# Kernel tuning notes

Hardware: AMD Instinct MI355X
Metric: run time of the kernel (lower is better)

The kernel has to match this reference:

```python
import jax, jax.numpy as jnp
import numpy as np

VOCAB, D = 10000, 32
QUEUE_LEN = 100


def setup_inputs() -> dict:
    key = jax.random.key(0)
    ks = jax.random.split(key, 8)
    B, T = 64, 1024
    s = 0.1
    return dict(
        inputs=jax.random.randint(ks[0], (B, T), 0, 10000, dtype=jnp.int32),
        emb=jax.random.normal(ks[1], (VOCAB, D), dtype=jnp.float32) * s,
        k_lstm=jax.random.normal(ks[2], (D, 4 * D), dtype=jnp.float32) * s,
        rk_lstm=jax.random.normal(ks[3], (D, 4 * D), dtype=jnp.float32) * s,
        b_lstm=jnp.zeros((4 * D,), dtype=jnp.float32),
        W1=jax.random.normal(ks[4], (D, D), dtype=jnp.float32) * s,
        b1=jnp.zeros((D,), dtype=jnp.float32),
        W2=jax.random.normal(ks[5], (D, 1), dtype=jnp.float32) * s,
        b2=jnp.zeros((1,), dtype=jnp.float32),
    )


def _lstm(x, k, rk, b):
    # Keras LSTM, gate order [i, f, g(cell), o], sigmoid recurrent act, tanh act.
    B, T, D = x.shape
    xg = jnp.einsum('btd,de->bte', x, k) + b  # precompute input projections

    def step(carry, xg_t):
        h, c = carry
        z = xg_t + h @ rk
        i, f, g, o = jnp.split(z, 4, axis=-1)
        c = jax.nn.sigmoid(f) * c + jax.nn.sigmoid(i) * jnp.tanh(g)
        h = jax.nn.sigmoid(o) * jnp.tanh(c)
        return (h, c), h

    init = (jnp.zeros((B, D), x.dtype), jnp.zeros((B, D), x.dtype))
    _, hs = jax.lax.scan(step, init, jnp.swapaxes(xg, 0, 1))  # [T,B,D]
    return jnp.swapaxes(hs, 0, 1)  # [B,T,D]


def _zero_index_queue(x_ids):
    # Vectorized replacement of the (i,j) Python scan: last QUEUE_LEN positions
    # (row-major order) where token==0, as [QUEUE_LEN,2] int32, padded with -1.
    B, T = x_ids.shape
    flat = (x_ids == 0).reshape(-1)
    N = flat.shape[0]
    ridx = jnp.nonzero(flat[::-1], size=QUEUE_LEN, fill_value=-1)[0]
    pos = jnp.where(ridx >= 0, N - 1 - ridx, -1)[::-1]  # ascending, like deque
    ii = jnp.where(pos >= 0, pos // T, -1)
    jj = jnp.where(pos >= 0, pos % T, -1)
    return jnp.stack([ii, jj], axis=-1).astype(jnp.int32)


def _forward_float(x_ids, emb, k_lstm, rk_lstm, b_lstm, W1, b1, W2, b2):
    x = emb[x_ids]                                  # [B,T,D]
    h = _lstm(x, k_lstm, rk_lstm, b_lstm)           # [B,T,D]
    scores = jnp.einsum('btd,bsd->bts', h, h)       # unscaled dot attention
    attn = jax.nn.softmax(scores, axis=-1)
    ctx = jnp.einsum('bts,bsd->btd', attn, h)       # Keras Attention output
    y = jnp.einsum('btd,bte->bde', ctx, h)          # Dot(axes=(1,1)) -> [B,D,D]
    y = jax.nn.relu(y @ W1 + b1)
    return jax.nn.sigmoid(y @ W2 + b2)              # [B,D,1]


def reference(inputs, emb, k_lstm, rk_lstm, b_lstm, W1, b1, W2, b2):
    x_ids = jnp.where(inputs < VOCAB, inputs, 0)
    out = _forward_float(x_ids, emb, k_lstm, rk_lstm, b_lstm, W1, b1, W2, b2)
    return out, _zero_index_queue(x_ids)
```

## Files before the change

kernel.cpp:

```cpp
#include <hip/hip_runtime.h>
#include <math.h>

#define BB 64
#define TT 1024
#define DD 32
#define GG 128
#define VOCABN 10000
#define QLEN 100

typedef short short8 __attribute__((ext_vector_type(8)));
typedef float floatx4 __attribute__((ext_vector_type(4)));
typedef float floatx2 __attribute__((ext_vector_type(2)));
typedef unsigned short u16;

__device__ __forceinline__ float fsig(float x) {
    return __builtin_amdgcn_rcpf(1.0f + __expf(-x));
}
__device__ __forceinline__ float readlane_f(float v, int l) {
    return __int_as_float(__builtin_amdgcn_readlane(__float_as_int(v), l));
}
__device__ __forceinline__ u16 f2bf_rne(float x) {
    unsigned u = __float_as_uint(x);
    u += 0x7FFF + ((u >> 16) & 1);
    return (u16)(u >> 16);
}
__device__ __forceinline__ float bf2f(u16 s) {
    return __uint_as_float(((unsigned)s) << 16);
}
__device__ __forceinline__ floatx2 fma2(float s, floatx2 w, floatx2 acc) {
    return __builtin_elementwise_fma((floatx2){s, s}, w, acc);
}

#define UU 8
__global__
__attribute__((amdgpu_flat_work_group_size(128, 128)))
__attribute__((amdgpu_waves_per_eu(1, 1)))
void k_lstm_scan(const int* __restrict__ ids,
                 const float* __restrict__ emb,
                 const float* __restrict__ klstm,
                 const float* __restrict__ bias,
                 const float* __restrict__ rk,
                 float* __restrict__ hout,
                 u16* __restrict__ hh, u16* __restrict__ hl,
                 u16* __restrict__ th, u16* __restrict__ tl,
                 int* __restrict__ list,
                 float* __restrict__ outq) {
    const int b = blockIdx.x;
    const int tid = threadIdx.x;
    const int wv = tid >> 6;
    const int l = tid & 63;
    if (b >= BB) {
        if (wv != 0) return;
        const int4* v4 = (const int4*)ids;
        const int C4 = (BB * TT) / 4 / 64;
        const int b4 = l * C4;
        int cnt = 0;
#pragma unroll 4
        for (int i = 0; i < C4; ++i) {
            int4 v = v4[b4 + i];
            cnt += (v.x == 0 || (unsigned)v.x >= VOCABN);
            cnt += (v.y == 0 || (unsigned)v.y >= VOCABN);
            cnt += (v.z == 0 || (unsigned)v.z >= VOCABN);
            cnt += (v.w == 0 || (unsigned)v.w >= VOCABN);
        }
        int scan = cnt;
#pragma unroll
        for (int o = 1; o < 64; o <<= 1) {
            int nn = __shfl_up(scan, o);
            if (l >= o) scan += nn;
        }
        const int total = __shfl(scan, 63);
        int off = scan - cnt;
        const int base = l * (C4 * 4);
#pragma unroll 4
        for (int i = 0; i < C4; ++i) {
            int4 v = v4[b4 + i];
            if (v.x == 0 || (unsigned)v.x >= VOCABN) list[off++] = base + 4 * i;
            if (v.y == 0 || (unsigned)v.y >= VOCABN) list[off++] = base + 4 * i + 1;
            if (v.z == 0 || (unsigned)v.z >= VOCABN) list[off++] = base + 4 * i + 2;
            if (v.w == 0 || (unsigned)v.w >= VOCABN) list[off++] = base + 4 * i + 3;
        }
        __threadfence();
        const int Kc = total < QLEN ? total : QLEN;
        for (int t = l; t < QLEN; t += 64) {
            float ii = -1.0f, jj = -1.0f;
            if (t >= QLEN - Kc) {
                int pos = list[total - QLEN + t];
                ii = (float)(pos >> 10);
                jj = (float)(pos & (TT - 1));
            }
            outq[2 * t] = ii;
            outq[2 * t + 1] = jj;
        }
        return;
    }

    __shared__ float ring[2][UU][GG];
    __shared__ __align__(16) float hring[2][UU][DD];
    const int* idsb = ids + b * TT;

    if (wv == 1) {
        const int ja = l, jb = l + 64;
        floatx2 kp[DD];
#pragma unroll
        for (int d2 = 0; d2 < DD; ++d2)
            kp[d2] = (floatx2){klstm[d2 * GG + ja], klstm[d2 * GG + jb]};
        const floatx2 bj = (floatx2){bias[ja], bias[jb]};
        const int dd = l & 31;
        const int u_r = l >> 3, dc = (l & 7) * 4;
        const int d_c = l & 31, ug = (l >> 5) * 4;
        u16* hhb = hh + (size_t)b * TT * DD;
        u16* hlb = hl + (size_t)b * TT * DD;
        u16* thb = th + (size_t)b * DD * TT;
        u16* tlb = tl + (size_t)b * DD * TT;

#define PROD_TOKEN(SEL, U, EV)                                               \
        {                                                                    \
            floatx2 z0 = bj;                                                 \
            floatx2 z1 = {0.f, 0.f}, z2 = {0.f, 0.f}, z3 = {0.f, 0.f};       \
            _Pragma("unroll")                                                \
            for (int k = 0; k < DD; k += 4) {                                \
                float e0 = readlane_f(EV, k);                                \
                float e1 = readlane_f(EV, k + 1);                            \
                float e2 = readlane_f(EV, k + 2);                            \
                float e3 = readlane_f(EV, k + 3);                            \
                z0 = fma2(e0, kp[k], z0);                                    \
                z1 = fma2(e1, kp[k + 1], z1);                                \
                z2 = fma2(e2, kp[k + 2], z2);                                \
                z3 = fma2(e3, kp[k + 3], z3);                                \
            }                                                                \
            floatx2 zf = (z0 + z1) + (z2 + z3);                              \
            ring[SEL][U][ja] = zf.x;                                         \
            ring[SEL][U][jb] = zf.y;                                         \
        }

#define CVT_CHUNK(HSEL, TC0)                                                 \
        {                                                                    \
            const float4 hv4 = *(const float4*)&hring[HSEL][u_r][dc];        \
            float xr[4] = {hv4.x, hv4.y, hv4.z, hv4.w};                      \
            u16 rh[4], rl[4];                                                \
            _Pragma("unroll")                                                \
            for (int i = 0; i < 4; ++i) {                                    \
                rh[i] = f2bf_rne(xr[i]);                                     \
                rl[i] = f2bf_rne(xr[i] - bf2f(rh[i]));                       \
            }                                                                \
            ushort4 rhv = {rh[0], rh[1], rh[2], rh[3]};                      \
            ushort4 rlv = {rl[0], rl[1], rl[2], rl[3]};                      \
            *(ushort4*)&hhb[(size_t)((TC0) + u_r) * DD + dc] = rhv;          \
            *(ushort4*)&hlb[(size_t)((TC0) + u_r) * DD + dc] = rlv;          \
            u16 ch[4], cl[4];                                                \
            _Pragma("unroll")                                                \
            for (int j = 0; j < 4; ++j) {                                    \
                float x = hring[HSEL][ug + j][d_c];                          \
                ch[j] = f2bf_rne(x);                                         \
                cl[j] = f2bf_rne(x - bf2f(ch[j]));                           \
            }                                                                \
            ushort4 chv = {ch[0], ch[1], ch[2], ch[3]};                      \
            ushort4 clv = {cl[0], cl[1], cl[2], cl[3]};                      \
            *(ushort4*)&thb[(size_t)d_c * TT + (TC0) + ug] = chv;            \
            *(ushort4*)&tlb[(size_t)d_c * TT + (TC0) + ug] = clv;            \
        }

        {
            int id0 = idsb[0]; if ((unsigned)id0 >= VOCABN) id0 = 0;
            float ec = emb[id0 * DD + dd];
#pragma unroll
            for (int u = 0; u < UU; ++u) {
                float en = 0.f;
                if (u + 1 < UU) {
                    int idn = idsb[u + 1]; if ((unsigned)idn >= VOCABN) idn = 0;
                    en = emb[idn * DD + dd];
                }
                PROD_TOKEN(0, u, ec)
                ec = en;
            }
        }
        __syncthreads();
        int sel = 0;
        for (int t0 = 0; t0 < TT; t0 += UU) {
            if (t0 + UU < TT) {
                const int s = sel ^ 1;
                int id0 = idsb[t0 + UU]; if ((unsigned)id0 >= VOCABN) id0 = 0;
                float ec = emb[id0 * DD + dd];
#pragma unroll
                for (int u = 0; u < UU; ++u) {
                    float en = 0.f;
                    if (u + 1 < UU) {
                        int tn = t0 + UU + u + 1;
                        if (tn > TT - 1) tn = TT - 1;
                        int idn = idsb[tn]; if ((unsigned)idn >= VOCABN) idn = 0;
                        en = emb[idn * DD + dd];
                    }
                    PROD_TOKEN(s, u, ec)
                    ec = en;
                }
            }
            if (t0) CVT_CHUNK((t0 / UU - 1) & 1, t0 - UU)
            __syncthreads();
            sel ^= 1;
        }
        CVT_CHUNK(1, TT - UU)
#undef PROD_TOKEN
#undef CVT_CHUNK
        return;
    }

    const int d = l & 31;
    const bool hi = l >= 32;
    const int ga = (hi ? 32 : 0) + d;
    const int gb = (hi ? 96 : 64) + d;
    floatx2 rkp[DD];
#pragma unroll
    for (int k = 0; k < DD; ++k)
        rkp[k] = (floatx2){rk[k * GG + ga], rk[k * GG + gb]};
    float* hb = hout + (size_t)b * TT * DD;

    float h = 0.0f, c = 0.0f;
    float hreg[UU];
    __syncthreads();
    int sel = 0;
    for (int t0 = 0; t0 < TT; t0 += UU) {
        if (t0 && !hi) {
#pragma unroll
            for (int u = 0; u < UU; ++u) hb[(size_t)(t0 - UU + u) * DD + d] = hreg[u];
        }
        float pa[UU], pb[UU];
#pragma unroll
        for (int u = 0; u < UU; ++u) {
            pa[u] = ring[sel][u][ga];
            pb[u] = ring[sel][u][gb];
        }
#pragma unroll
        for (int u = 0; u < UU; ++u) {
            floatx2 x0 = {pa[u], pb[u]};
            floatx2 x1 = {0.f, 0.f}, x2 = {0.f, 0.f}, x3 = {0.f, 0.f};
#pragma unroll
            for (int k = 0; k < DD; k += 4) {
                float h0 = readlane_f(h, k);
                float h1 = readlane_f(h, k + 1);
                float h2 = readlane_f(h, k + 2);
                float h3 = readlane_f(h, k + 3);
                x0 = fma2(h0, rkp[k],     x0);
                x1 = fma2(h1, rkp[k + 1], x1);
                x2 = fma2(h2, rkp[k + 2], x2);
                x3 = fma2(h3, rkp[k + 3], x3);
            }
            floatx2 zf = (x0 + x1) + (x2 + x3);
            float za = zf.x, zb = zf.y;
            float a = fsig(za);
            float zbm = hi ? zb : 2.0f * zb;
            float s2 = fsig(zbm);
            float bv = hi ? s2 : 2.0f * s2 - 1.0f;
            auto r1 = __builtin_amdgcn_permlane32_swap(
                __float_as_int(bv), __float_as_int(a), false, false);
            auto r2 = __builtin_amdgcn_permlane32_swap(
                __float_as_int(a), __float_as_int(bv), false, false);
            float fg = __int_as_float(r1[0]);
            float og = __int_as_float(r2[0]);
            c = fmaf(fg, c, a * bv);
            float tc = 2.0f * fsig(2.0f * c) - 1.0f;
            h = og * tc;
            hreg[u] = h;
            if (!hi) hring[sel][u][d] = h;
        }
        __syncthreads();
        sel ^= 1;
    }
    if (!hi) {
#pragma unroll
        for (int u = 0; u < UU; ++u) hb[(size_t)(TT - UU + u) * DD + d] = hreg[u];
    }
}

__global__ __launch_bounds__(256, 1) void k_attn(const u16* __restrict__ hh,
                                                 const u16* __restrict__ hl,
                                                 const u16* __restrict__ th,
                                                 const u16* __restrict__ tl,
                                                 u16* __restrict__ cth,
                                                 u16* __restrict__ ctl) {
    __shared__ u16 plds[4][4][2][16 * 40];
    const int tid = threadIdx.x;
    const int w = tid >> 6;
    const int l = tid & 63;
    const int m = l & 15;
    const int g = l >> 4;
    const int b = blockIdx.x & 63;
    const int qt = (blockIdx.x >> 6) * 4 + w;
    const int q0 = qt * 64;
    const size_t rb = (size_t)b * TT * DD;
    const size_t tb = (size_t)b * DD * TT;

    const short8 Qh0 = *(const short8*)&hh[rb + (size_t)(q0 + m) * DD + g * 8];
    const short8 Ql0 = *(const short8*)&hl[rb + (size_t)(q0 + m) * DD + g * 8];
    const short8 Qh1 = *(const short8*)&hh[rb + (size_t)(q0 + 16 + m) * DD + g * 8];
    const short8 Ql1 = *(const short8*)&hl[rb + (size_t)(q0 + 16 + m) * DD + g * 8];
    const short8 Qh2 = *(const short8*)&hh[rb + (size_t)(q0 + 32 + m) * DD + g * 8];
    const short8 Ql2 = *(const short8*)&hl[rb + (size_t)(q0 + 32 + m) * DD + g * 8];
    const short8 Qh3 = *(const short8*)&hh[rb + (size_t)(q0 + 48 + m) * DD + g * 8];
    const short8 Ql3 = *(const short8*)&hl[rb + (size_t)(q0 + 48 + m) * DD + g * 8];
    short8 ONES;
#pragma unroll
    for (int j = 0; j < 8; ++j) ONES[j] = (short)0x3F80;

    floatx4 c0 = {0.f, 0.f, 0.f, 0.f}, c1 = {0.f, 0.f, 0.f, 0.f};
    floatx4 c2 = {0.f, 0.f, 0.f, 0.f}, c3 = {0.f, 0.f, 0.f, 0.f};
    floatx4 c4 = {0.f, 0.f, 0.f, 0.f}, c5 = {0.f, 0.f, 0.f, 0.f};
    floatx4 c6 = {0.f, 0.f, 0.f, 0.f}, c7 = {0.f, 0.f, 0.f, 0.f};
    floatx4 la0 = {0.f, 0.f, 0.f, 0.f}, la1 = {0.f, 0.f, 0.f, 0.f};
    floatx4 la2 = {0.f, 0.f, 0.f, 0.f}, la3 = {0.f, 0.f, 0.f, 0.f};

#define S_BLOCK(QH, QL, KH_A, KL_A, KH_B, KL_B, SA, SB)                       \
    SA = __builtin_amdgcn_mfma_f32_16x16x32_bf16(QH, KH_A, SA, 0, 0, 0);      \
    SA = __builtin_amdgcn_mfma_f32_16x16x32_bf16(QH, KL_A, SA, 0, 0, 0);      \
    SA = __builtin_amdgcn_mfma_f32_16x16x32_bf16(QL, KH_A, SA, 0, 0, 0);      \
    SB = __builtin_amdgcn_mfma_f32_16x16x32_bf16(QH, KH_B, SB, 0, 0, 0);      \
    SB = __builtin_amdgcn_mfma_f32_16x16x32_bf16(QH, KL_B, SB, 0, 0, 0);      \
    SB = __builtin_amdgcn_mfma_f32_16x16x32_bf16(QL, KH_B, SB, 0, 0, 0);

#define EXP_STORE(SA, SB, TILE, SLOT)                                         \
    {                                                                         \
        u16* lp = plds[w][TILE][SLOT];                                        \
        _Pragma("unroll")                                                     \
        for (int r = 0; r < 4; ++r) {                                         \
            lp[(g * 4 + r) * 40 + m]      = f2bf_rne(__expf(SA[r]));          \
            lp[(g * 4 + r) * 40 + 16 + m] = f2bf_rne(__expf(SB[r]));          \
        }                                                                     \
    }

    {
        short8 KhA = *(const short8*)&hh[rb + (size_t)(m) * DD + g * 8];
        short8 KlA = *(const short8*)&hl[rb + (size_t)(m) * DD + g * 8];
        short8 KhB = *(const short8*)&hh[rb + (size_t)(16 + m) * DD + g * 8];
        short8 KlB = *(const short8*)&hl[rb + (size_t)(16 + m) * DD + g * 8];
        floatx4 sA = {0.f, 0.f, 0.f, 0.f}, sB = {0.f, 0.f, 0.f, 0.f};
        floatx4 tA = {0.f, 0.f, 0.f, 0.f}, tB = {0.f, 0.f, 0.f, 0.f};
        floatx4 uA = {0.f, 0.f, 0.f, 0.f}, uB = {0.f, 0.f, 0.f, 0.f};
        floatx4 vA = {0.f, 0.f, 0.f, 0.f}, vB = {0.f, 0.f, 0.f, 0.f};
        S_BLOCK(Qh0, Ql0, KhA, KlA, KhB, KlB, sA, sB)
        S_BLOCK(Qh1, Ql1, KhA, KlA, KhB, KlB, tA, tB)
        S_BLOCK(Qh2, Ql2, KhA, KlA, KhB, KlB, uA, uB)
        S_BLOCK(Qh3, Ql3, KhA, KlA, KhB, KlB, vA, vB)
        EXP_STORE(sA, sB, 0, 0)
        EXP_STORE(tA, tB, 1, 0)
        EXP_STORE(uA, uB, 2, 0)
        EXP_STORE(vA, vB, 3, 0)
    }
    short8 Vh0 = *(const short8*)&th[tb + (size_t)m * TT + g * 8];
    short8 Vl0 = *(const short8*)&tl[tb + (size_t)m * TT + g * 8];
    short8 Vh1 = *(const short8*)&th[tb + (size_t)(16 + m) * TT + g * 8];
    short8 Vl1 = *(const short8*)&tl[tb + (size_t)(16 + m) * TT + g * 8];
    short8 KhA = *(const short8*)&hh[rb + (size_t)(32 + m) * DD + g * 8];
    short8 KlA = *(const short8*)&hl[rb + (size_t)(32 + m) * DD + g * 8];
    short8 KhB = *(const short8*)&hh[rb + (size_t)(48 + m) * DD + g * 8];
    short8 KlB = *(const short8*)&hl[rb + (size_t)(48 + m) * DD + g * 8];

#pragma unroll 1
    for (int kp = 1; kp < 32; ++kp) {
        const int knK = (kp < 31) ? (kp + 1) * 32 : 0;
        const int knV = kp * 32;
        short8 nKhA = *(const short8*)&hh[rb + (size_t)(knK + m) * DD + g * 8];
        short8 nKlA = *(const short8*)&hl[rb + (size_t)(knK + m) * DD + g * 8];
        short8 nKhB = *(const short8*)&hh[rb + (size_t)(knK + 16 + m) * DD + g * 8];
        short8 nKlB = *(const short8*)&hl[rb + (size_t)(knK + 16 + m) * DD + g * 8];
        short8 nVh0 = *(const short8*)&th[tb + (size_t)m * TT + knV + g * 8];
        short8 nVl0 = *(const short8*)&tl[tb + (size_t)m * TT + knV + g * 8];
        short8 nVh1 = *(const short8*)&th[tb + (size_t)(16 + m) * TT + knV + g * 8];
        short8 nVl1 = *(const short8*)&tl[tb + (size_t)(16 + m) * TT + knV + g * 8];

        floatx4 sA = {0.f, 0.f, 0.f, 0.f}, sB = {0.f, 0.f, 0.f, 0.f};
        floatx4 tA = {0.f, 0.f, 0.f, 0.f}, tB = {0.f, 0.f, 0.f, 0.f};
        floatx4 uA = {0.f, 0.f, 0.f, 0.f}, uB = {0.f, 0.f, 0.f, 0.f};
        floatx4 vA = {0.f, 0.f, 0.f, 0.f}, vB = {0.f, 0.f, 0.f, 0.f};
        S_BLOCK(Qh0, Ql0, KhA, KlA, KhB, KlB, sA, sB)
        S_BLOCK(Qh1, Ql1, KhA, KlA, KhB, KlB, tA, tB)
        S_BLOCK(Qh2, Ql2, KhA, KlA, KhB, KlB, uA, uB)
        S_BLOCK(Qh3, Ql3, KhA, KlA, KhB, KlB, vA, vB)

        const int ps = (kp - 1) & 1;
        const short8 P0 = *(const short8*)&plds[w][0][ps][m * 40 + g * 8];
        const short8 P1 = *(const short8*)&plds[w][1][ps][m * 40 + g * 8];
        const short8 P2 = *(const short8*)&plds[w][2][ps][m * 40 + g * 8];
        const short8 P3 = *(const short8*)&plds[w][3][ps][m * 40 + g * 8];

        c0  = __builtin_amdgcn_mfma_f32_16x16x32_bf16(P0, Vh0, c0, 0, 0, 0);
        c0  = __builtin_amdgcn_mfma_f32_16x16x32_bf16(P0, Vl0, c0, 0, 0, 0);
        c1  = __builtin_amdgcn_mfma_f32_16x16x32_bf16(P0, Vh1, c1, 0, 0, 0);
        c1  = __builtin_amdgcn_mfma_f32_16x16x32_bf16(P0, Vl1, c1, 0, 0, 0);
        la0 = __builtin_amdgcn_mfma_f32_16x16x32_bf16(P0, ONES, la0, 0, 0, 0);
        c2  = __builtin_amdgcn_mfma_f32_16x16x32_bf16(P1, Vh0, c2, 0, 0, 0);
        c2  = __builtin_amdgcn_mfma_f32_16x16x32_bf16(P1, Vl0, c2, 0, 0, 0);
        c3  = __builtin_amdgcn_mfma_f32_16x16x32_bf16(P1, Vh1, c3, 0, 0, 0);
        c3  = __builtin_amdgcn_mfma_f32_16x16x32_bf16(P1, Vl1, c3, 0, 0, 0);
        la1 = __builtin_amdgcn_mfma_f32_16x16x32_bf16(P1, ONES, la1, 0, 0, 0);
        c4  = __builtin_amdgcn_mfma_f32_16x16x32_bf16(P2, Vh0, c4, 0, 0, 0);
        c4  = __builtin_amdgcn_mfma_f32_16x16x32_bf16(P2, Vl0, c4, 0, 0, 0);
        c5  = __builtin_amdgcn_mfma_f32_16x16x32_bf16(P2, Vh1, c5, 0, 0, 0);
        c5  = __builtin_amdgcn_mfma_f32_16x16x32_bf16(P2, Vl1, c5, 0, 0, 0);
        la2 = __builtin_amdgcn_mfma_f32_16x16x32_bf16(P2, ONES, la2, 0, 0, 0);
        c6  = __builtin_amdgcn_mfma_f32_16x16x32_bf16(P3, Vh0, c6, 0, 0, 0);
        c6  = __builtin_amdgcn_mfma_f32_16x16x32_bf16(P3, Vl0, c6, 0, 0, 0);
        c7  = __builtin_amdgcn_mfma_f32_16x16x32_bf16(P3, Vh1, c7, 0, 0, 0);
        c7  = __builtin_amdgcn_mfma_f32_16x16x32_bf16(P3, Vl1, c7, 0, 0, 0);
        la3 = __builtin_amdgcn_mfma_f32_16x16x32_bf16(P3, ONES, la3, 0, 0, 0);

        EXP_STORE(sA, sB, 0, kp & 1)
        EXP_STORE(tA, tB, 1, kp & 1)
        EXP_STORE(uA, uB, 2, kp & 1)
        EXP_STORE(vA, vB, 3, kp & 1)

        KhA = nKhA; KlA = nKlA; KhB = nKhB; KlB = nKlB;
        Vh0 = nVh0; Vl0 = nVl0; Vh1 = nVh1; Vl1 = nVl1;
    }
    {
        const short8 P0 = *(const short8*)&plds[w][0][1][m * 40 + g * 8];
        const short8 P1 = *(const short8*)&plds[w][1][1][m * 40 + g * 8];
        const short8 P2 = *(const short8*)&plds[w][2][1][m * 40 + g * 8];
        const short8 P3 = *(const short8*)&plds[w][3][1][m * 40 + g * 8];
        c0  = __builtin_amdgcn_mfma_f32_16x16x32_bf16(P0, Vh0, c0, 0, 0, 0);
        c0  = __builtin_amdgcn_mfma_f32_16x16x32_bf16(P0, Vl0, c0, 0, 0, 0);
        c1  = __builtin_amdgcn_mfma_f32_16x16x32_bf16(P0, Vh1, c1, 0, 0, 0);
        c1  = __builtin_amdgcn_mfma_f32_16x16x32_bf16(P0, Vl1, c1, 0, 0, 0);
        la0 = __builtin_amdgcn_mfma_f32_16x16x32_bf16(P0, ONES, la0, 0, 0, 0);
        c2  = __builtin_amdgcn_mfma_f32_16x16x32_bf16(P1, Vh0, c2, 0, 0, 0);
        c2  = __builtin_amdgcn_mfma_f32_16x16x32_bf16(P1, Vl0, c2, 0, 0, 0);
        c3  = __builtin_amdgcn_mfma_f32_16x16x32_bf16(P1, Vh1, c3, 0, 0, 0);
        c3  = __builtin_amdgcn_mfma_f32_16x16x32_bf16(P1, Vl1, c3, 0, 0, 0);
        la1 = __builtin_amdgcn_mfma_f32_16x16x32_bf16(P1, ONES, la1, 0, 0, 0);
        c4  = __builtin_amdgcn_mfma_f32_16x16x32_bf16(P2, Vh0, c4, 0, 0, 0);
        c4  = __builtin_amdgcn_mfma_f32_16x16x32_bf16(P2, Vl0, c4, 0, 0, 0);
        c5  = __builtin_amdgcn_mfma_f32_16x16x32_bf16(P2, Vh1, c5, 0, 0, 0);
        c5  = __builtin_amdgcn_mfma_f32_16x16x32_bf16(P2, Vl1, c5, 0, 0, 0);
        la2 = __builtin_amdgcn_mfma_f32_16x16x32_bf16(P2, ONES, la2, 0, 0, 0);
        c6  = __builtin_amdgcn_mfma_f32_16x16x32_bf16(P3, Vh0, c6, 0, 0, 0);
        c6  = __builtin_amdgcn_mfma_f32_16x16x32_bf16(P3, Vl0, c6, 0, 0, 0);
        c7  = __builtin_amdgcn_mfma_f32_16x16x32_bf16(P3, Vh1, c7, 0, 0, 0);
        c7  = __builtin_amdgcn_mfma_f32_16x16x32_bf16(P3, Vl1, c7, 0, 0, 0);
        la3 = __builtin_amdgcn_mfma_f32_16x16x32_bf16(P3, ONES, la3, 0, 0, 0);
    }
#undef S_BLOCK
#undef EXP_STORE
#define CTX_STORE(VAL, DROW, TCOL)                                            \
    {                                                                         \
        float v_ = (VAL);                                                     \
        u16 h_ = f2bf_rne(v_);                                                \
        cth[tb + (size_t)(DROW) * TT + (TCOL)] = h_;                          \
        ctl[tb + (size_t)(DROW) * TT + (TCOL)] = f2bf_rne(v_ - bf2f(h_));     \
    }
#pragma unroll
    for (int r = 0; r < 4; ++r) {
        float li0 = __builtin_amdgcn_rcpf(la0[r]);
        float li1 = __builtin_amdgcn_rcpf(la1[r]);
        float li2 = __builtin_amdgcn_rcpf(la2[r]);
        float li3 = __builtin_amdgcn_rcpf(la3[r]);
        const int ta = q0 + g * 4 + r;
        const int tbr = q0 + 16 + g * 4 + r;
        const int tc = q0 + 32 + g * 4 + r;
        const int td = q0 + 48 + g * 4 + r;
        CTX_STORE(c0[r] * li0, m, ta)
        CTX_STORE(c1[r] * li0, 16 + m, ta)
        CTX_STORE(c2[r] * li1, m, tbr)
        CTX_STORE(c3[r] * li1, 16 + m, tbr)
        CTX_STORE(c4[r] * li2, m, tc)
        CTX_STORE(c5[r] * li2, 16 + m, tc)
        CTX_STORE(c6[r] * li3, m, td)
        CTX_STORE(c7[r] * li3, 16 + m, td)
    }
#undef CTX_STORE
}

__global__ __launch_bounds__(256) void k_ymlp(const u16* __restrict__ cth,
                                              const u16* __restrict__ ctl,
                                              const u16* __restrict__ th,
                                              const u16* __restrict__ tl,
                                              const float* __restrict__ W1,
                                              const float* __restrict__ b1,
                                              const float* __restrict__ W2,
                                              const float* __restrict__ b2,
                                              float* __restrict__ out) {
    const int b = blockIdx.x;
    const int tid = threadIdx.x;
    const int w = tid >> 6;
    const int l = tid & 63;
    const int m = l & 15;
    const int g = l >> 4;
    const size_t tb = (size_t)b * DD * TT;
    const int k0 = w * (TT / 4);

    floatx4 y00 = {0.f, 0.f, 0.f, 0.f}, y01 = {0.f, 0.f, 0.f, 0.f};
    floatx4 y10 = {0.f, 0.f, 0.f, 0.f}, y11 = {0.f, 0.f, 0.f, 0.f};
#pragma unroll 2
    for (int ks = 0; ks < TT / 4; ks += 32) {
        const size_t kk = (size_t)(k0 + ks + g * 8);
        short8 A0h = *(const short8*)&cth[tb + (size_t)m * TT + kk];
        short8 A0l = *(const short8*)&ctl[tb + (size_t)m * TT + kk];
        short8 A1h = *(const short8*)&cth[tb + (size_t)(16 + m) * TT + kk];
        short8 A1l = *(const short8*)&ctl[tb + (size_t)(16 + m) * TT + kk];
        short8 B0h = *(const short8*)&th[tb + (size_t)m * TT + kk];
        short8 B0l = *(const short8*)&tl[tb + (size_t)m * TT + kk];
        short8 B1h = *(const short8*)&th[tb + (size_t)(16 + m) * TT + kk];
        short8 B1l = *(const short8*)&tl[tb + (size_t)(16 + m) * TT + kk];
        y00 = __builtin_amdgcn_mfma_f32_16x16x32_bf16(A0h, B0h, y00, 0, 0, 0);
        y00 = __builtin_amdgcn_mfma_f32_16x16x32_bf16(A0h, B0l, y00, 0, 0, 0);
        y00 = __builtin_amdgcn_mfma_f32_16x16x32_bf16(A0l, B0h, y00, 0, 0, 0);
        y01 = __builtin_amdgcn_mfma_f32_16x16x32_bf16(A0h, B1h, y01, 0, 0, 0);
        y01 = __builtin_amdgcn_mfma_f32_16x16x32_bf16(A0h, B1l, y01, 0, 0, 0);
        y01 = __builtin_amdgcn_mfma_f32_16x16x32_bf16(A0l, B1h, y01, 0, 0, 0);
        y10 = __builtin_amdgcn_mfma_f32_16x16x32_bf16(A1h, B0h, y10, 0, 0, 0);
        y10 = __builtin_amdgcn_mfma_f32_16x16x32_bf16(A1h, B0l, y10, 0, 0, 0);
        y10 = __builtin_amdgcn_mfma_f32_16x16x32_bf16(A1l, B0h, y10, 0, 0, 0);
        y11 = __builtin_amdgcn_mfma_f32_16x16x32_bf16(A1h, B1h, y11, 0, 0, 0);
        y11 = __builtin_amdgcn_mfma_f32_16x16x32_bf16(A1h, B1l, y11, 0, 0, 0);
        y11 = __builtin_amdgcn_mfma_f32_16x16x32_bf16(A1l, B1h, y11, 0, 0, 0);
    }
    __shared__ float ysp[4][DD][DD];
#pragma unroll
    for (int r = 0; r < 4; ++r) {
        ysp[w][g * 4 + r][m]           = y00[r];
        ysp[w][g * 4 + r][16 + m]      = y01[r];
        ysp[w][16 + g * 4 + r][m]      = y10[r];
        ysp[w][16 + g * 4 + r][16 + m] = y11[r];
    }
    __syncthreads();
    const int e = tid & 31;
    const int d4 = (tid >> 5) * 4;
    __shared__ float ys[DD][DD];
#pragma unroll
    for (int r = 0; r < 4; ++r)
        ys[d4 + r][e] = (ysp[0][d4 + r][e] + ysp[1][d4 + r][e])
                      + (ysp[2][d4 + r][e] + ysp[3][d4 + r][e]);
    __syncthreads();
    __shared__ float yr[DD][33];
#pragma unroll
    for (int r = 0; r < 4; ++r) {
        float v = b1[e];
#pragma unroll
        for (int ee = 0; ee < DD; ++ee) v += ys[d4 + r][ee] * W1[ee * DD + e];
        yr[d4 + r][e] = fmaxf(v, 0.0f);
    }
    __syncthreads();
    if (tid < DD) {
        float v = b2[0];
#pragma unroll
        for (int ee = 0; ee < DD; ++ee) v += yr[tid][ee] * W2[ee];
        out[b * DD + tid] = 1.0f / (1.0f + expf(-v));
    }
}

extern "C" void kernel_launch(void* const* d_in, const int* in_sizes, int n_in,
                              void* d_out, int out_size, void* d_ws, size_t ws_size,
                              hipStream_t stream) {
    const int* ids   = (const int*)d_in[0];
    const float* emb = (const float*)d_in[1];
    const float* kl  = (const float*)d_in[2];
    const float* rk  = (const float*)d_in[3];
    const float* bl  = (const float*)d_in[4];
    const float* W1  = (const float*)d_in[5];
    const float* b1  = (const float*)d_in[6];
    const float* W2  = (const float*)d_in[7];
    const float* b2  = (const float*)d_in[8];
    float* out = (float*)d_out;

    char* ws = (char*)d_ws;
    const size_t H_ELEMS = (size_t)BB * TT * DD;
    u16* hh   = (u16*)ws;
    u16* hl   = (u16*)(ws + H_ELEMS * 2);
    u16* th   = (u16*)(ws + H_ELEMS * 4);
    u16* tl   = (u16*)(ws + H_ELEMS * 6);
    float* h  = (float*)(ws + H_ELEMS * 8);
    u16* cth  = (u16*)(ws + H_ELEMS * 8 + H_ELEMS * 4);
    u16* ctl  = (u16*)(ws + H_ELEMS * 8 + H_ELEMS * 4 + H_ELEMS * 2);
    int* list = (int*)(ws + H_ELEMS * 8 + H_ELEMS * 8);

    k_lstm_scan<<<BB + 1, 128, 0, stream>>>(ids, emb, kl, bl, rk, h,
                                            hh, hl, th, tl, list, out + BB * DD);
    k_attn<<<BB * 4, 256, 0, stream>>>(hh, hl, th, tl, cth, ctl);
    k_ymlp<<<BB, 256, 0, stream>>>(cth, ctl, th, tl, W1, b1, W2, b2, out);
}
```

Before: 366.5 us.

## Deepen K/V prefetch to two iterations and stage ctx stores through LDS

The attention kernel now prefetches K tiles two iterations ahead and V tiles one iteration ahead, adding an extra register stage, so global load latency is better hidden behind the MFMA work. The context output is first written to a per-wave LDS tile in fp32 and then transposed, so each lane can write 16-byte vectorized bf16 hi/lo stores instead of scattered 2-byte stores. The cost is higher register pressure from the extra prefetch buffers, roughly 34KB of extra shared memory, and an extra LDS round trip in the epilogue.

```diff
diff --git a/kernel.cpp b/kernel.cpp
--- a/kernel.cpp
+++ b/kernel.cpp
@@ -279,6 +279,7 @@
                                                  u16* __restrict__ cth,
                                                  u16* __restrict__ ctl) {
     __shared__ u16 plds[4][4][2][16 * 40];
+    __shared__ float ctile[4][64][34];
     const int tid = threadIdx.x;
     const int w = tid >> 6;
     const int l = tid & 63;
@@ -349,15 +350,23 @@
     short8 Vl0 = *(const short8*)&tl[tb + (size_t)m * TT + g * 8];
     short8 Vh1 = *(const short8*)&th[tb + (size_t)(16 + m) * TT + g * 8];
     short8 Vl1 = *(const short8*)&tl[tb + (size_t)(16 + m) * TT + g * 8];
+    short8 V2h0 = *(const short8*)&th[tb + (size_t)m * TT + 32 + g * 8];
+    short8 V2l0 = *(const short8*)&tl[tb + (size_t)m * TT + 32 + g * 8];
+    short8 V2h1 = *(const short8*)&th[tb + (size_t)(16 + m) * TT + 32 + g * 8];
+    short8 V2l1 = *(const short8*)&tl[tb + (size_t)(16 + m) * TT + 32 + g * 8];
     short8 KhA = *(const short8*)&hh[rb + (size_t)(32 + m) * DD + g * 8];
     short8 KlA = *(const short8*)&hl[rb + (size_t)(32 + m) * DD + g * 8];
     short8 KhB = *(const short8*)&hh[rb + (size_t)(48 + m) * DD + g * 8];
     short8 KlB = *(const short8*)&hl[rb + (size_t)(48 + m) * DD + g * 8];
+    short8 K2hA = *(const short8*)&hh[rb + (size_t)(64 + m) * DD + g * 8];
+    short8 K2lA = *(const short8*)&hl[rb + (size_t)(64 + m) * DD + g * 8];
+    short8 K2hB = *(const short8*)&hh[rb + (size_t)(80 + m) * DD + g * 8];
+    short8 K2lB = *(const short8*)&hl[rb + (size_t)(80 + m) * DD + g * 8];
 
 #pragma unroll 1
     for (int kp = 1; kp < 32; ++kp) {
-        const int knK = (kp < 31) ? (kp + 1) * 32 : 0;
-        const int knV = kp * 32;
+        const int knK = (kp < 30) ? (kp + 2) * 32 : 0;
+        const int knV = (kp < 31) ? (kp + 1) * 32 : 0;
         short8 nKhA = *(const short8*)&hh[rb + (size_t)(knK + m) * DD + g * 8];
         short8 nKlA = *(const short8*)&hl[rb + (size_t)(knK + m) * DD + g * 8];
         short8 nKhB = *(const short8*)&hh[rb + (size_t)(knK + 16 + m) * DD + g * 8];
@@ -408,8 +417,10 @@
         EXP_STORE(uA, uB, 2, kp & 1)
         EXP_STORE(vA, vB, 3, kp & 1)
 
-        KhA = nKhA; KlA = nKlA; KhB = nKhB; KlB = nKlB;
-        Vh0 = nVh0; Vl0 = nVl0; Vh1 = nVh1; Vl1 = nVl1;
+        KhA = K2hA; KlA = K2lA; KhB = K2hB; KlB = K2lB;
+        K2hA = nKhA; K2lA = nKlA; K2hB = nKhB; K2lB = nKlB;
+        Vh0 = V2h0; Vl0 = V2l0; Vh1 = V2h1; Vl1 = V2l1;
+        V2h0 = nVh0; V2l0 = nVl0; V2h1 = nVh1; V2l1 = nVl1;
     }
     {
         const short8 P0 = *(const short8*)&plds[w][0][1][m * 40 + g * 8];
@@ -439,33 +450,37 @@
     }
 #undef S_BLOCK
 #undef EXP_STORE
-#define CTX_STORE(VAL, DROW, TCOL)                                            \
-    {                                                                         \
-        float v_ = (VAL);                                                     \
-        u16 h_ = f2bf_rne(v_);                                                \
-        cth[tb + (size_t)(DROW) * TT + (TCOL)] = h_;                          \
-        ctl[tb + (size_t)(DROW) * TT + (TCOL)] = f2bf_rne(v_ - bf2f(h_));     \
-    }
 #pragma unroll
     for (int r = 0; r < 4; ++r) {
         float li0 = __builtin_amdgcn_rcpf(la0[r]);
         float li1 = __builtin_amdgcn_rcpf(la1[r]);
         float li2 = __builtin_amdgcn_rcpf(la2[r]);
         float li3 = __builtin_amdgcn_rcpf(la3[r]);
-        const int ta = q0 + g * 4 + r;
-        const int tbr = q0 + 16 + g * 4 + r;
-        const int tc = q0 + 32 + g * 4 + r;
-        const int td = q0 + 48 + g * 4 + r;
-        CTX_STORE(c0[r] * li0, m, ta)
-        CTX_STORE(c1[r] * li0, 16 + m, ta)
-        CTX_STORE(c2[r] * li1, m, tbr)
-        CTX_STORE(c3[r] * li1, 16 + m, tbr)
-        CTX_STORE(c4[r] * li2, m, tc)
-        CTX_STORE(c5[r] * li2, 16 + m, tc)
-        CTX_STORE(c6[r] * li3, m, td)
-        CTX_STORE(c7[r] * li3, 16 + m, td)
-    }
-#undef CTX_STORE
+        ctile[w][g * 4 + r][m]            = c0[r] * li0;
+        ctile[w][g * 4 + r][16 + m]       = c1[r] * li0;
+        ctile[w][16 + g * 4 + r][m]       = c2[r] * li1;
+        ctile[w][16 + g * 4 + r][16 + m]  = c3[r] * li1;
+        ctile[w][32 + g * 4 + r][m]       = c4[r] * li2;
+        ctile[w][32 + g * 4 + r][16 + m]  = c5[r] * li2;
+        ctile[w][48 + g * 4 + r][m]       = c6[r] * li3;
+        ctile[w][48 + g * 4 + r][16 + m]  = c7[r] * li3;
+    }
+    const int srow = l >> 3;
+    const int tcol = (l & 7) * 8;
+#pragma unroll
+    for (int cblk = 0; cblk < 4; ++cblk) {
+        const int dr = cblk * 8 + srow;
+        short8 hvec, lvec;
+#pragma unroll
+        for (int j2 = 0; j2 < 8; ++j2) {
+            float v = ctile[w][tcol + j2][dr];
+            u16 hv = f2bf_rne(v);
+            hvec[j2] = (short)hv;
+            lvec[j2] = (short)f2bf_rne(v - bf2f(hv));
+        }
+        *(short8*)&cth[tb + (size_t)dr * TT + q0 + tcol] = hvec;
+        *(short8*)&ctl[tb + (size_t)dr * TT + q0 + tcol] = lvec;
+    }
 }
 
 __global__ __launch_bounds__(256) void k_ymlp(const u16* __restrict__ cth,
```

Result: faster. 358.1 us (-2.3%).
